# Performance work log

Measured on AMD Instinct MI355X. Metric: run time of the kernel, lower is better.

## Reference

```python
import jax, jax.numpy as jnp
import numpy as np
from jax import lax

K = 3        # kernel size
PAD = 1      # padding
K2 = K * K


def conv2d(x, w, b):
    # x: [B,C,H,W], w: [O,C,K,K], b: [O]
    y = lax.conv_general_dilated(
        x, w, window_strides=(1, 1), padding=((PAD, PAD), (PAD, PAD)),
        dimension_numbers=("NCHW", "OIHW", "NCHW"))
    return y + b[None, :, None, None]


def bilinear_sample(img, py, px):
    # img: [C,H,W]; py, px: [K2,H,W] float sampling coords (zero padding outside)
    H, W = img.shape[1], img.shape[2]
    y0 = jnp.floor(py); x0 = jnp.floor(px)
    wy1 = py - y0; wx1 = px - x0
    wy0 = 1.0 - wy1; wx0 = 1.0 - wx1

    def gather(yi, xi, wgt):
        yc = jnp.clip(yi, 0, H - 1).astype(jnp.int32)
        xc = jnp.clip(xi, 0, W - 1).astype(jnp.int32)
        valid = ((yi >= 0) & (yi <= H - 1) & (xi >= 0) & (xi <= W - 1))
        v = img[:, yc, xc]                      # [C,K2,H,W]
        return v * (wgt * valid.astype(img.dtype))[None]

    return (gather(y0, x0, wy0 * wx0) + gather(y0, x0 + 1, wy0 * wx1)
            + gather(y0 + 1, x0, wy1 * wx0) + gather(y0 + 1, x0 + 1, wy1 * wx1))


def deform_conv2d(x, offset, weight, bias):
    # x: [B,C,H,W], offset: [B,2*K2,H,W] as (dy,dx) pairs per kernel tap
    B, C, H, W = x.shape
    off = offset.reshape(B, K2, 2, H, W)
    ks_y = (jnp.arange(K2) // K - PAD).astype(x.dtype)   # kernel tap y offsets
    ks_x = (jnp.arange(K2) % K - PAD).astype(x.dtype)
    base_y = ks_y[:, None, None] + jnp.arange(H, dtype=x.dtype)[None, :, None]
    base_x = ks_x[:, None, None] + jnp.arange(W, dtype=x.dtype)[None, None, :]
    py = off[:, :, 0] + base_y                            # [B,K2,H,W]
    px = off[:, :, 1] + base_x
    sampled = jax.vmap(bilinear_sample)(x, py, px)        # [B,C,K2,H,W]
    out = jnp.einsum("bckhw,ock->bohw", sampled, weight.reshape(weight.shape[0], C, K2))
    return out + bias[None, :, None, None]


def setup_inputs() -> dict:
    key = jax.random.key(0)
    ks = jax.random.split(key, 5)
    B, C, O, H, W = 4, 64, 64, 128, 128
    s_off = 1.0 / np.sqrt(C * K2)
    return {
        "x": jax.random.normal(ks[0], (B, C, H, W), dtype=jnp.float32),
        "w_off": jax.random.normal(ks[1], (2 * K2, C, K, K), dtype=jnp.float32) * s_off,
        "b_off": jnp.zeros((2 * K2,), dtype=jnp.float32),
        "weight": jax.random.normal(ks[2], (O, C, K, K), dtype=jnp.float32) * s_off,
        "bias": jax.random.normal(ks[3], (O,), dtype=jnp.float32) * 0.01,
    }


def reference(x, w_off, b_off, weight, bias):
    offset = conv2d(x, w_off, b_off)          # [B,18,H,W]
    return deform_conv2d(x, offset, weight, bias)
```

## Files before the change

kernel.cpp:

```cpp
#include <hip/hip_runtime.h>
#include <hip/hip_bf16.h>

#define BB 4
#define CC 64
#define OO 64
#define HH 128
#define WW 128
#define HW (HH * WW)
#define K2 9
#define OCOFF 18
#define SMP_STRIDE 36

typedef __attribute__((ext_vector_type(8))) short short8;
typedef __attribute__((ext_vector_type(16))) float f32x16;

__device__ __forceinline__ unsigned short bf16_rne(float v) {
  unsigned u = __builtin_bit_cast(unsigned, v);
  return (unsigned short)((u + 0x7FFFu + ((u >> 16) & 1u)) >> 16);
}
__device__ __forceinline__ void bf16_split(float v, unsigned short& hi, unsigned short& lo) {
  hi = bf16_rne(v);
  float hf = __builtin_bit_cast(float, (unsigned)hi << 16);
  lo = bf16_rne(v - hf);
}
__device__ __forceinline__ float4 ld4(const float* p) { return *(const float4*)p; }

__global__ __launch_bounds__(256) void prep_wfrag(
    const float* __restrict__ weight, unsigned* __restrict__ wf) {
  int d = blockIdx.x * 256 + threadIdx.x;
  if (d >= 9 * 4096) return;
  int j2 = d & 3, l = (d >> 2) & 63, hh = (d >> 8) & 1, s = (d >> 9) & 3,
      m = (d >> 11) & 1, c = d >> 12;
  int o = m * 32 + (l & 31);
  int g = l >> 5;
  int ch0 = s * 16 + g * 8 + j2 * 2;
  float v0 = weight[(o * 64 + ch0) * 9 + c];
  float v1 = weight[(o * 64 + ch0 + 1) * 9 + c];
  unsigned short h0, l0, h1, l1;
  bf16_split(v0, h0, l0);
  bf16_split(v1, h1, l1);
  unsigned short b0 = hh ? l0 : h0;
  unsigned short b1 = hh ? l1 : h1;
  wf[d] = (unsigned)b0 | ((unsigned)b1 << 16);
}

__global__ __launch_bounds__(256) void prep_wofrag(
    const float* __restrict__ w_off, unsigned* __restrict__ wof) {
  int d = blockIdx.x * 256 + threadIdx.x;
  if (d >= 9 * 2048) return;
  int j2 = d & 3, l = (d >> 2) & 63, hh = (d >> 8) & 1, s = (d >> 9) & 3,
      c = d >> 11;
  int oc = l & 31;
  int g = l >> 5;
  int ch0 = s * 16 + g * 8 + j2 * 2;
  unsigned r = 0;
  if (oc < OCOFF) {
    float v0 = w_off[(oc * 64 + ch0) * 9 + c];
    float v1 = w_off[(oc * 64 + ch0 + 1) * 9 + c];
    unsigned short h0, l0, h1, l1;
    bf16_split(v0, h0, l0);
    bf16_split(v1, h1, l1);
    unsigned short b0 = hh ? l0 : h0;
    unsigned short b1 = hh ? l1 : h1;
    r = (unsigned)b0 | ((unsigned)b1 << 16);
  }
  wof[d] = r;
}

__global__ __launch_bounds__(256) void transpose_x(
    const float* __restrict__ x, float* __restrict__ xt) {
  __shared__ float tile[64][33];
  int blk = blockIdx.x;
  int wt = blk & 3, h = (blk >> 2) & 127, b = blk >> 9;
  int w0 = wt * 32;
  int t = threadIdx.x;
  {
    int w_l = t & 31, c_l = t >> 5;
#pragma unroll
    for (int i = 0; i < 8; ++i) {
      int cc = c_l * 8 + i;
      tile[cc][w_l] = x[(((size_t)b * 64 + cc) * 128 + h) * 128 + w0 + w_l];
    }
  }
  __syncthreads();
  {
    int c_w = t & 63, w_w = t >> 6;
#pragma unroll
    for (int i = 0; i < 8; ++i) {
      int wl = w_w * 8 + i;
      xt[(((size_t)b * 128 + h) * 128 + w0 + wl) * 64 + c_w] = tile[c_w][wl];
    }
  }
}

struct TapD { int o00, o01, o10, o11; float w00, w01, w10, w11; };

__device__ __forceinline__ TapD mk_tapd(float oyv, float oxv, int h, int wpix, int kk) {
  TapD t;
  const int dy = kk / 3 - 1, dx = kk - (kk / 3) * 3 - 1;
  float py = oyv + (float)(h + dy);
  float px = oxv + (float)(wpix + dx);
  float y0f = floorf(py), x0f = floorf(px);
  float wy1 = py - y0f, wx1 = px - x0f;
  float wy0 = 1.0f - wy1, wx0 = 1.0f - wx1;
  int y0 = (int)y0f, x0 = (int)x0f, y1 = y0 + 1, x1 = x0 + 1;
  bool vy0 = (unsigned)y0 < (unsigned)HH, vy1 = (unsigned)y1 < (unsigned)HH;
  bool vx0 = (unsigned)x0 < (unsigned)WW, vx1 = (unsigned)x1 < (unsigned)WW;
  t.w00 = (vy0 && vx0) ? wy0 * wx0 : 0.0f;
  t.w01 = (vy0 && vx1) ? wy0 * wx1 : 0.0f;
  t.w10 = (vy1 && vx0) ? wy1 * wx0 : 0.0f;
  t.w11 = (vy1 && vx1) ? wy1 * wx1 : 0.0f;
  int y0c = min(max(y0, 0), HH - 1), y1c = min(max(y1, 0), HH - 1);
  int x0c = min(max(x0, 0), WW - 1), x1c = min(max(x1, 0), WW - 1);
  t.o00 = (y0c * WW + x0c) * CC;
  t.o01 = (y0c * WW + x1c) * CC;
  t.o10 = (y1c * WW + x0c) * CC;
  t.o11 = (y1c * WW + x1c) * CC;
  return t;
}

struct TapO { int ofs; float vf; };

__device__ __forceinline__ TapO mk_tapo(int h, int wpix, int kk) {
  TapO t;
  const int dy = kk / 3 - 1, dx = kk - (kk / 3) * 3 - 1;
  int y = h + dy, x = wpix + dx;
  bool v = ((unsigned)y < (unsigned)HH) && ((unsigned)x < (unsigned)WW);
  t.vf = v ? 1.0f : 0.0f;
  int yc = min(max(y, 0), HH - 1), xc = min(max(x, 0), WW - 1);
  t.ofs = (yc * WW + xc) * CC;
  return t;
}

__device__ __forceinline__ void issueD(float4 (&st)[8], const float* xb,
                                       const TapD& t, int j4) {
  st[0] = ld4(xb + t.o00 + j4);      st[1] = ld4(xb + t.o01 + j4);
  st[2] = ld4(xb + t.o10 + j4);      st[3] = ld4(xb + t.o11 + j4);
  st[4] = ld4(xb + t.o00 + 32 + j4); st[5] = ld4(xb + t.o01 + 32 + j4);
  st[6] = ld4(xb + t.o10 + 32 + j4); st[7] = ld4(xb + t.o11 + 32 + j4);
}
__device__ __forceinline__ void issueO(float4 (&st)[2], const float* xb,
                                       const TapO& t, int j4) {
  st[0] = ld4(xb + t.ofs + j4);
  st[1] = ld4(xb + t.ofs + 32 + j4);
}

__device__ __forceinline__ void pack_write(unsigned* mh, unsigned* ml,
                                           int pl, int j, int hf,
                                           const float v[4]) {
  unsigned short h0, l0, h1, l1, h2, l2, h3, l3;
  bf16_split(v[0], h0, l0); bf16_split(v[1], h1, l1);
  bf16_split(v[2], h2, l2); bf16_split(v[3], h3, l3);
  int idx = pl * SMP_STRIDE + hf * 16 + j * 2;
  *(uint2*)&mh[idx] = make_uint2((unsigned)h0 | ((unsigned)h1 << 16),
                                 (unsigned)h2 | ((unsigned)h3 << 16));
  *(uint2*)&ml[idx] = make_uint2((unsigned)l0 | ((unsigned)l1 << 16),
                                 (unsigned)l2 | ((unsigned)l3 << 16));
}

__device__ __forceinline__ void consumeD(unsigned* mh, unsigned* ml,
                                         int pl, int j,
                                         const float4 (&st)[8], const TapD& t) {
#pragma unroll
  for (int hf = 0; hf < 2; ++hf) {
    float v[4];
#pragma unroll
    for (int q = 0; q < 4; ++q)
      v[q] = fmaf(t.w00, st[hf * 4 + 0][q], fmaf(t.w01, st[hf * 4 + 1][q],
             fmaf(t.w10, st[hf * 4 + 2][q], t.w11 * st[hf * 4 + 3][q])));
    pack_write(mh, ml, pl, j, hf, v);
  }
}

__device__ __forceinline__ void consumeO(unsigned* mh, unsigned* ml,
                                         int pl, int j,
                                         const float4 (&st)[2], const TapO& t) {
#pragma unroll
  for (int hf = 0; hf < 2; ++hf) {
    float v[4];
#pragma unroll
    for (int q = 0; q < 4; ++q) v[q] = t.vf * st[hf][q];
    pack_write(mh, ml, pl, j, hf, v);
  }
}

__global__ __launch_bounds__(128, 2) void fused_deform(
    const float* __restrict__ xt, const unsigned* __restrict__ wfrag,
    const unsigned* __restrict__ wofrag, const float* __restrict__ b_off,
    const float* __restrict__ bias, float* __restrict__ out) {
  __shared__ __align__(16) unsigned smph[2][32 * SMP_STRIDE];
  __shared__ __align__(16) unsigned smpl[2][32 * SMP_STRIDE];
  __shared__ __align__(16) float offs_lds[2][32 * OCOFF];

  const int blk = blockIdx.x;
  const int sx = (blk & 7) * 128 + (blk >> 3);
  const int seg = sx & 1, h = (sx >> 1) & 127, b = sx >> 8;
  const int tid = threadIdx.x;
  const int l = tid & 63, wv = tid >> 6;
  const int P = l & 31, g = l >> 5;
  const int j = l & 7, pq = l >> 3;
  const int j4 = j * 4;
  const int wbase = seg * 64 + wv * 32;

  const float* xb = xt + (size_t)b * HW * CC;
  unsigned* mh = smph[wv];
  unsigned* ml = smpl[wv];
  float* ol = offs_lds[wv];

  {
    f32x16 accO = {0,0,0,0,0,0,0,0,0,0,0,0,0,0,0,0};
    TapO tA, tB;
    float4 sA[2], sB[2];
    tA = mk_tapo(h, wbase + pq, 0);
    issueO(sA, xb, tA, j4);
#pragma unroll
    for (int c = 0; c < 9; ++c) {
      tB = mk_tapo(h, wbase + 8 + pq, c);
      issueO(sB, xb, tB, j4);
      consumeO(mh, ml, pq, j, sA, tA);
      tA = mk_tapo(h, wbase + 16 + pq, c);
      issueO(sA, xb, tA, j4);
      consumeO(mh, ml, 8 + pq, j, sB, tB);
      tB = mk_tapo(h, wbase + 24 + pq, c);
      issueO(sB, xb, tB, j4);
      consumeO(mh, ml, 16 + pq, j, sA, tA);
      if (c < 8) {
        tA = mk_tapo(h, wbase + pq, c + 1);
        issueO(sA, xb, tA, j4);
      }
      consumeO(mh, ml, 24 + pq, j, sB, tB);
#pragma unroll
      for (int s = 0; s < 4; ++s) {
        int ridx = P * SMP_STRIDE + s * 8 + g * 4;
        short8 sh8 = *(const short8*)&mh[ridx];
        short8 sl8 = *(const short8*)&ml[ridx];
        const unsigned* wb = wofrag + ((size_t)((c * 8 + s * 2) * 64 + l)) * 4;
        short8 wh = *(const short8*)(wb);
        short8 wl = *(const short8*)(wb + 256);
        accO = __builtin_amdgcn_mfma_f32_32x32x16_bf16(wh, sh8, accO, 0, 0, 0);
        accO = __builtin_amdgcn_mfma_f32_32x32x16_bf16(wh, sl8, accO, 0, 0, 0);
        accO = __builtin_amdgcn_mfma_f32_32x32x16_bf16(wl, sh8, accO, 0, 0, 0);
      }
    }
#pragma unroll
    for (int r = 0; r < 16; ++r) {
      int oc = (r & 3) + 8 * (r >> 2) + 4 * g;
      if (oc < OCOFF) ol[P * OCOFF + oc] = accO[r] + b_off[oc];
    }
  }

  f32x16 acc0 = {0,0,0,0,0,0,0,0,0,0,0,0,0,0,0,0};
  f32x16 acc1 = {0,0,0,0,0,0,0,0,0,0,0,0,0,0,0,0};
  {
    TapD tA, tB;
    float4 sA[8], sB[8];
    {
      float2 o = *(const float2*)&ol[pq * OCOFF + 0];
      tA = mk_tapd(o.x, o.y, h, wbase + pq, 0);
      issueD(sA, xb, tA, j4);
    }
#pragma unroll
    for (int c = 0; c < 9; ++c) {
      {
        float2 o = *(const float2*)&ol[(8 + pq) * OCOFF + 2 * c];
        tB = mk_tapd(o.x, o.y, h, wbase + 8 + pq, c);
        issueD(sB, xb, tB, j4);
      }
      consumeD(mh, ml, pq, j, sA, tA);
      {
        float2 o = *(const float2*)&ol[(16 + pq) * OCOFF + 2 * c];
        tA = mk_tapd(o.x, o.y, h, wbase + 16 + pq, c);
        issueD(sA, xb, tA, j4);
      }
      consumeD(mh, ml, 8 + pq, j, sB, tB);
      {
        float2 o = *(const float2*)&ol[(24 + pq) * OCOFF + 2 * c];
        tB = mk_tapd(o.x, o.y, h, wbase + 24 + pq, c);
        issueD(sB, xb, tB, j4);
      }
      consumeD(mh, ml, 16 + pq, j, sA, tA);
      if (c < 8) {
        float2 o = *(const float2*)&ol[pq * OCOFF + 2 * (c + 1)];
        tA = mk_tapd(o.x, o.y, h, wbase + pq, c + 1);
        issueD(sA, xb, tA, j4);
      }
      consumeD(mh, ml, 24 + pq, j, sB, tB);
#pragma unroll
      for (int s = 0; s < 4; ++s) {
        int ridx = P * SMP_STRIDE + s * 8 + g * 4;
        short8 sh8 = *(const short8*)&mh[ridx];
        short8 sl8 = *(const short8*)&ml[ridx];
        const unsigned* wb = wfrag + ((size_t)((c * 16 + s * 2) * 64 + l)) * 4;
        short8 wh0 = *(const short8*)(wb);
        short8 wl0 = *(const short8*)(wb + 256);
        short8 wh1 = *(const short8*)(wb + 2048);
        short8 wl1 = *(const short8*)(wb + 2304);
        acc0 = __builtin_amdgcn_mfma_f32_32x32x16_bf16(wh0, sh8, acc0, 0, 0, 0);
        acc0 = __builtin_amdgcn_mfma_f32_32x32x16_bf16(wh0, sl8, acc0, 0, 0, 0);
        acc0 = __builtin_amdgcn_mfma_f32_32x32x16_bf16(wl0, sh8, acc0, 0, 0, 0);
        acc1 = __builtin_amdgcn_mfma_f32_32x32x16_bf16(wh1, sh8, acc1, 0, 0, 0);
        acc1 = __builtin_amdgcn_mfma_f32_32x32x16_bf16(wh1, sl8, acc1, 0, 0, 0);
        acc1 = __builtin_amdgcn_mfma_f32_32x32x16_bf16(wl1, sh8, acc1, 0, 0, 0);
      }
    }
  }

  const int wpix = wbase + P;
#pragma unroll
  for (int r = 0; r < 16; ++r) {
    int o0 = (r & 3) + 8 * (r >> 2) + 4 * g;
    out[(((size_t)b * 64 + o0) * 128 + h) * 128 + wpix] = acc0[r] + bias[o0];
    out[(((size_t)b * 64 + 32 + o0) * 128 + h) * 128 + wpix] = acc1[r] + bias[32 + o0];
  }
}

extern "C" void kernel_launch(void* const* d_in, const int* in_sizes, int n_in,
                              void* d_out, int out_size, void* d_ws, size_t ws_size,
                              hipStream_t stream) {
  const float* x      = (const float*)d_in[0];
  const float* w_off  = (const float*)d_in[1];
  const float* b_off  = (const float*)d_in[2];
  const float* weight = (const float*)d_in[3];
  const float* bias   = (const float*)d_in[4];
  float* out = (float*)d_out;

  float*    xt     = (float*)d_ws;
  unsigned* wfrag  = (unsigned*)(xt + (size_t)4194304);
  unsigned* wofrag = wfrag + 36864;

  prep_wfrag<<<144, 256, 0, stream>>>(weight, wfrag);
  prep_wofrag<<<72, 256, 0, stream>>>(w_off, wofrag);
  transpose_x<<<2048, 256, 0, stream>>>(x, xt);

  fused_deform<<<1024, 128, 0, stream>>>(xt, wfrag, wofrag, b_off, bias, out);
}
```

Measured before the change: 150.3 us.

## Merge prep kernels, load offset-conv operands directly into registers, use packed bf16 convert

```diff
diff --git a/kernel.cpp b/kernel.cpp
--- a/kernel.cpp
+++ b/kernel.cpp
@@ -14,6 +14,22 @@
 typedef __attribute__((ext_vector_type(8))) short short8;
 typedef __attribute__((ext_vector_type(16))) float f32x16;
 
+union U8 { unsigned u[4]; short8 s8; };
+
+__device__ __forceinline__ float uf(unsigned u) { return __builtin_bit_cast(float, u); }
+
+__device__ __forceinline__ unsigned cvtpk(float a, float b) {
+  unsigned r;
+  asm("v_cvt_pk_bf16_f32 %0, %1, %2" : "=v"(r) : "v"(a), "v"(b));
+  return r;
+}
+__device__ __forceinline__ void split2(float a, float b, unsigned& ph, unsigned& pl) {
+  ph = cvtpk(a, b);
+  float ra = a - uf(ph << 16);
+  float rb = b - uf(ph & 0xFFFF0000u);
+  pl = cvtpk(ra, rb);
+}
+
 __device__ __forceinline__ unsigned short bf16_rne(float v) {
   unsigned u = __builtin_bit_cast(unsigned, v);
   return (unsigned short)((u + 0x7FFFu + ((u >> 16) & 1u)) >> 16);
@@ -25,71 +41,74 @@
 }
 __device__ __forceinline__ float4 ld4(const float* p) { return *(const float4*)p; }
 
-__global__ __launch_bounds__(256) void prep_wfrag(
-    const float* __restrict__ weight, unsigned* __restrict__ wf) {
-  int d = blockIdx.x * 256 + threadIdx.x;
-  if (d >= 9 * 4096) return;
-  int j2 = d & 3, l = (d >> 2) & 63, hh = (d >> 8) & 1, s = (d >> 9) & 3,
-      m = (d >> 11) & 1, c = d >> 12;
-  int o = m * 32 + (l & 31);
-  int g = l >> 5;
-  int ch0 = s * 16 + g * 8 + j2 * 2;
-  float v0 = weight[(o * 64 + ch0) * 9 + c];
-  float v1 = weight[(o * 64 + ch0 + 1) * 9 + c];
-  unsigned short h0, l0, h1, l1;
-  bf16_split(v0, h0, l0);
-  bf16_split(v1, h1, l1);
-  unsigned short b0 = hh ? l0 : h0;
-  unsigned short b1 = hh ? l1 : h1;
-  wf[d] = (unsigned)b0 | ((unsigned)b1 << 16);
-}
-
-__global__ __launch_bounds__(256) void prep_wofrag(
-    const float* __restrict__ w_off, unsigned* __restrict__ wof) {
-  int d = blockIdx.x * 256 + threadIdx.x;
-  if (d >= 9 * 2048) return;
-  int j2 = d & 3, l = (d >> 2) & 63, hh = (d >> 8) & 1, s = (d >> 9) & 3,
-      c = d >> 11;
-  int oc = l & 31;
-  int g = l >> 5;
-  int ch0 = s * 16 + g * 8 + j2 * 2;
-  unsigned r = 0;
-  if (oc < OCOFF) {
-    float v0 = w_off[(oc * 64 + ch0) * 9 + c];
-    float v1 = w_off[(oc * 64 + ch0 + 1) * 9 + c];
+__global__ __launch_bounds__(256) void prep_all(
+    const float* __restrict__ x, const float* __restrict__ weight,
+    const float* __restrict__ w_off, float* __restrict__ xt,
+    unsigned* __restrict__ wf, unsigned* __restrict__ wof) {
+  int blk = blockIdx.x;
+  int t = threadIdx.x;
+  if (blk < 2048) {
+    __shared__ float tile[64][33];
+    int wt = blk & 3, h = (blk >> 2) & 127, b = blk >> 9;
+    int w0 = wt * 32;
+    {
+      int w_l = t & 31, c_l = t >> 5;
+#pragma unroll
+      for (int i = 0; i < 8; ++i) {
+        int cc = c_l * 8 + i;
+        tile[cc][w_l] = x[(((size_t)b * 64 + cc) * 128 + h) * 128 + w0 + w_l];
+      }
+    }
+    __syncthreads();
+    {
+      int c_w = t & 63, w_w = t >> 6;
+#pragma unroll
+      for (int i = 0; i < 8; ++i) {
+        int wl = w_w * 8 + i;
+        xt[(((size_t)b * 128 + h) * 128 + w0 + wl) * 64 + c_w] = tile[c_w][wl];
+      }
+    }
+    return;
+  }
+  if (blk < 2048 + 144) {
+    int d = (blk - 2048) * 256 + t;
+    if (d >= 9 * 4096) return;
+    int j2 = d & 3, l = (d >> 2) & 63, hh = (d >> 8) & 1, s = (d >> 9) & 3,
+        m = (d >> 11) & 1, c = d >> 12;
+    int o = m * 32 + (l & 31);
+    int g = l >> 5;
+    int ch0 = s * 16 + g * 8 + j2 * 2;
+    float v0 = weight[(o * 64 + ch0) * 9 + c];
+    float v1 = weight[(o * 64 + ch0 + 1) * 9 + c];
     unsigned short h0, l0, h1, l1;
     bf16_split(v0, h0, l0);
     bf16_split(v1, h1, l1);
     unsigned short b0 = hh ? l0 : h0;
     unsigned short b1 = hh ? l1 : h1;
-    r = (unsigned)b0 | ((unsigned)b1 << 16);
-  }
-  wof[d] = r;
-}
-
-__global__ __launch_bounds__(256) void transpose_x(
-    const float* __restrict__ x, float* __restrict__ xt) {
-  __shared__ float tile[64][33];
-  int blk = blockIdx.x;
-  int wt = blk & 3, h = (blk >> 2) & 127, b = blk >> 9;
-  int w0 = wt * 32;
-  int t = threadIdx.x;
+    wf[d] = (unsigned)b0 | ((unsigned)b1 << 16);
+    return;
+  }
   {
-    int w_l = t & 31, c_l = t >> 5;
-#pragma unroll
-    for (int i = 0; i < 8; ++i) {
-      int cc = c_l * 8 + i;
-      tile[cc][w_l] = x[(((size_t)b * 64 + cc) * 128 + h) * 128 + w0 + w_l];
-    }
-  }
-  __syncthreads();
-  {
-    int c_w = t & 63, w_w = t >> 6;
-#pragma unroll
-    for (int i = 0; i < 8; ++i) {
-      int wl = w_w * 8 + i;
-      xt[(((size_t)b * 128 + h) * 128 + w0 + wl) * 64 + c_w] = tile[c_w][wl];
-    }
+    int d = (blk - 2192) * 256 + t;
+    if (d >= 9 * 2048) return;
+    int j2 = d & 3, l = (d >> 2) & 63, hh = (d >> 8) & 1, s = (d >> 9) & 3,
+        c = d >> 11;
+    int oc = l & 31;
+    int g = l >> 5;
+    int ch0 = s * 16 + g * 8 + j2 * 2;
+    unsigned r = 0;
+    if (oc < OCOFF) {
+      float v0 = w_off[(oc * 64 + ch0) * 9 + c];
+      float v1 = w_off[(oc * 64 + ch0 + 1) * 9 + c];
+      unsigned short h0, l0, h1, l1;
+      bf16_split(v0, h0, l0);
+      bf16_split(v1, h1, l1);
+      unsigned short b0 = hh ? l0 : h0;
+      unsigned short b1 = hh ? l1 : h1;
+      r = (unsigned)b0 | ((unsigned)b1 << 16);
+    }
+    wof[d] = r;
+    return;
   }
 }
 
@@ -119,19 +138,6 @@
   return t;
 }
 
-struct TapO { int ofs; float vf; };
-
-__device__ __forceinline__ TapO mk_tapo(int h, int wpix, int kk) {
-  TapO t;
-  const int dy = kk / 3 - 1, dx = kk - (kk / 3) * 3 - 1;
-  int y = h + dy, x = wpix + dx;
-  bool v = ((unsigned)y < (unsigned)HH) && ((unsigned)x < (unsigned)WW);
-  t.vf = v ? 1.0f : 0.0f;
-  int yc = min(max(y, 0), HH - 1), xc = min(max(x, 0), WW - 1);
-  t.ofs = (yc * WW + xc) * CC;
-  return t;
-}
-
 __device__ __forceinline__ void issueD(float4 (&st)[8], const float* xb,
                                        const TapD& t, int j4) {
   st[0] = ld4(xb + t.o00 + j4);      st[1] = ld4(xb + t.o01 + j4);
@@ -139,24 +145,6 @@
   st[4] = ld4(xb + t.o00 + 32 + j4); st[5] = ld4(xb + t.o01 + 32 + j4);
   st[6] = ld4(xb + t.o10 + 32 + j4); st[7] = ld4(xb + t.o11 + 32 + j4);
 }
-__device__ __forceinline__ void issueO(float4 (&st)[2], const float* xb,
-                                       const TapO& t, int j4) {
-  st[0] = ld4(xb + t.ofs + j4);
-  st[1] = ld4(xb + t.ofs + 32 + j4);
-}
-
-__device__ __forceinline__ void pack_write(unsigned* mh, unsigned* ml,
-                                           int pl, int j, int hf,
-                                           const float v[4]) {
-  unsigned short h0, l0, h1, l1, h2, l2, h3, l3;
-  bf16_split(v[0], h0, l0); bf16_split(v[1], h1, l1);
-  bf16_split(v[2], h2, l2); bf16_split(v[3], h3, l3);
-  int idx = pl * SMP_STRIDE + hf * 16 + j * 2;
-  *(uint2*)&mh[idx] = make_uint2((unsigned)h0 | ((unsigned)h1 << 16),
-                                 (unsigned)h2 | ((unsigned)h3 << 16));
-  *(uint2*)&ml[idx] = make_uint2((unsigned)l0 | ((unsigned)l1 << 16),
-                                 (unsigned)l2 | ((unsigned)l3 << 16));
-}
 
 __device__ __forceinline__ void consumeD(unsigned* mh, unsigned* ml,
                                          int pl, int j,
@@ -168,19 +156,12 @@
     for (int q = 0; q < 4; ++q)
       v[q] = fmaf(t.w00, st[hf * 4 + 0][q], fmaf(t.w01, st[hf * 4 + 1][q],
              fmaf(t.w10, st[hf * 4 + 2][q], t.w11 * st[hf * 4 + 3][q])));
-    pack_write(mh, ml, pl, j, hf, v);
-  }
-}
-
-__device__ __forceinline__ void consumeO(unsigned* mh, unsigned* ml,
-                                         int pl, int j,
-                                         const float4 (&st)[2], const TapO& t) {
-#pragma unroll
-  for (int hf = 0; hf < 2; ++hf) {
-    float v[4];
-#pragma unroll
-    for (int q = 0; q < 4; ++q) v[q] = t.vf * st[hf][q];
-    pack_write(mh, ml, pl, j, hf, v);
+    unsigned h01, l01, h23, l23;
+    split2(v[0], v[1], h01, l01);
+    split2(v[2], v[3], h23, l23);
+    int idx = pl * SMP_STRIDE + hf * 16 + j * 2;
+    *(uint2*)&mh[idx] = make_uint2(h01, h23);
+    *(uint2*)&ml[idx] = make_uint2(l01, l23);
   }
 }
 
@@ -209,37 +190,33 @@
 
   {
     f32x16 accO = {0,0,0,0,0,0,0,0,0,0,0,0,0,0,0,0};
-    TapO tA, tB;
-    float4 sA[2], sB[2];
-    tA = mk_tapo(h, wbase + pq, 0);
-    issueO(sA, xb, tA, j4);
 #pragma unroll
     for (int c = 0; c < 9; ++c) {
-      tB = mk_tapo(h, wbase + 8 + pq, c);
-      issueO(sB, xb, tB, j4);
-      consumeO(mh, ml, pq, j, sA, tA);
-      tA = mk_tapo(h, wbase + 16 + pq, c);
-      issueO(sA, xb, tA, j4);
-      consumeO(mh, ml, 8 + pq, j, sB, tB);
-      tB = mk_tapo(h, wbase + 24 + pq, c);
-      issueO(sB, xb, tB, j4);
-      consumeO(mh, ml, 16 + pq, j, sA, tA);
-      if (c < 8) {
-        tA = mk_tapo(h, wbase + pq, c + 1);
-        issueO(sA, xb, tA, j4);
-      }
-      consumeO(mh, ml, 24 + pq, j, sB, tB);
+      const int dy = c / 3 - 1, dx = c - (c / 3) * 3 - 1;
+      const int y = h + dy;
+      const int xp = wbase + P + dx;
+      const bool valid = ((unsigned)y < (unsigned)HH) && ((unsigned)xp < (unsigned)WW);
+      const unsigned msk = valid ? 0xFFFFFFFFu : 0u;
+      const int yc = min(max(y, 0), HH - 1), xc = min(max(xp, 0), WW - 1);
+      const unsigned* rowp = (const unsigned*)(xb + (size_t)(yc * WW + xc) * CC);
 #pragma unroll
       for (int s = 0; s < 4; ++s) {
-        int ridx = P * SMP_STRIDE + s * 8 + g * 4;
-        short8 sh8 = *(const short8*)&mh[ridx];
-        short8 sl8 = *(const short8*)&ml[ridx];
+        const int cb = s * 16 + g * 8;
+        uint4 u0 = *(const uint4*)(rowp + cb);
+        uint4 u1 = *(const uint4*)(rowp + cb + 4);
+        u0.x &= msk; u0.y &= msk; u0.z &= msk; u0.w &= msk;
+        u1.x &= msk; u1.y &= msk; u1.z &= msk; u1.w &= msk;
+        U8 sh, sl;
+        split2(uf(u0.x), uf(u0.y), sh.u[0], sl.u[0]);
+        split2(uf(u0.z), uf(u0.w), sh.u[1], sl.u[1]);
+        split2(uf(u1.x), uf(u1.y), sh.u[2], sl.u[2]);
+        split2(uf(u1.z), uf(u1.w), sh.u[3], sl.u[3]);
         const unsigned* wb = wofrag + ((size_t)((c * 8 + s * 2) * 64 + l)) * 4;
         short8 wh = *(const short8*)(wb);
         short8 wl = *(const short8*)(wb + 256);
-        accO = __builtin_amdgcn_mfma_f32_32x32x16_bf16(wh, sh8, accO, 0, 0, 0);
-        accO = __builtin_amdgcn_mfma_f32_32x32x16_bf16(wh, sl8, accO, 0, 0, 0);
-        accO = __builtin_amdgcn_mfma_f32_32x32x16_bf16(wl, sh8, accO, 0, 0, 0);
+        accO = __builtin_amdgcn_mfma_f32_32x32x16_bf16(wh, sh.s8, accO, 0, 0, 0);
+        accO = __builtin_amdgcn_mfma_f32_32x32x16_bf16(wh, sl.s8, accO, 0, 0, 0);
+        accO = __builtin_amdgcn_mfma_f32_32x32x16_bf16(wl, sh.s8, accO, 0, 0, 0);
       }
     }
 #pragma unroll
@@ -328,9 +305,6 @@
   unsigned* wfrag  = (unsigned*)(xt + (size_t)4194304);
   unsigned* wofrag = wfrag + 36864;
 
-  prep_wfrag<<<144, 256, 0, stream>>>(weight, wfrag);
-  prep_wofrag<<<72, 256, 0, stream>>>(w_off, wofrag);
-  transpose_x<<<2048, 256, 0, stream>>>(x, xt);
-
+  prep_all<<<2264, 256, 0, stream>>>(x, weight, w_off, xt, wfrag, wofrag);
   fused_deform<<<1024, 128, 0, stream>>>(xt, wfrag, wofrag, b_off, bias, out);
 }
```

New measurement: 146.5 us. 2.5% less time.
